# Performance work log

Hardware: AMD Instinct MI355X
Metric: run time of the kernel (lower is better)

The kernel has to match this reference:

```python
import jax, jax.numpy as jnp
import numpy as np

B, S, D, H = 2, 4096, 768, 12
DK = D // H

def setup_inputs() -> dict:
    key = jax.random.key(0)
    ks = jax.random.split(key, 11)
    scale = 1.0 / np.sqrt(D)
    inp = {
        'q': jax.random.normal(ks[0], (B, S, D), jnp.float32),
        'k': jax.random.normal(ks[1], (B, S, D), jnp.float32),
        'v': jax.random.normal(ks[2], (B, S, D), jnp.float32),
        'wq': jax.random.normal(ks[3], (D, D), jnp.float32) * scale,
        'bq': jnp.zeros((D,), jnp.float32),
        'wk': jax.random.normal(ks[4], (D, D), jnp.float32) * scale,
        'bk': jnp.zeros((D,), jnp.float32),
        'wv': jax.random.normal(ks[5], (D, D), jnp.float32) * scale,
        'bv': jnp.zeros((D,), jnp.float32),
        'wo': jax.random.normal(ks[6], (D, D), jnp.float32) * scale,
        'bo': jnp.zeros((D,), jnp.float32),
        # causal mask [S, S]; code path: 2D mask -> broadcast over batch & heads
        'mask': jnp.tril(jnp.ones((S, S), dtype=bool)),
    }
    return inp

def reference(q, k, v, wq, bq, wk, bk, wv, bv, wo, bo, mask):
    # torch Linear: y = x @ W.T + b
    def proj(x, w, b):
        # [B,S,D] -> [B,H,S,DK]
        y = jnp.einsum('bsd,ed->bse', x, w) + b
        return y.reshape(B, S, H, DK).transpose(0, 2, 1, 3)
    Q, K, V = proj(q, wq, bq), proj(k, wk, bk), proj(v, wv, bv)
    scores = jnp.einsum('bhqd,bhkd->bhqk', Q, K) / np.sqrt(DK)  # [B,H,S,S]
    scores = jnp.where(mask[None, None, :, :], scores, -1e9)
    probs = jax.nn.softmax(scores, axis=-1)
    ctx = jnp.einsum('bhqk,bhkd->bhqd', probs, V)  # [B,H,S,DK]
    ctx = ctx.transpose(0, 2, 1, 3).reshape(B, S, D)
    return jnp.einsum('bsd,ed->bse', ctx, wo) + bo
```

## Files before the change

### kernel.cpp

```cpp
#include <hip/hip_runtime.h>
#include <hip/hip_bf16.h>
#include <stdint.h>

typedef __bf16 bf16_t;
typedef __attribute__((ext_vector_type(8))) __bf16 bf16x8;
typedef __attribute__((ext_vector_type(4))) float f32x4;
typedef __attribute__((ext_vector_type(16))) float f32x16;
typedef __attribute__((ext_vector_type(2))) unsigned u32x2;

#define MFMA16(a,b,c) __builtin_amdgcn_mfma_f32_16x16x32_bf16((a),(b),(c),0,0,0)
#define MFMA32(a,b,c) __builtin_amdgcn_mfma_f32_32x32x16_bf16((a),(b),(c),0,0,0)

constexpr int BATCH = 2, SEQ = 4096, DMODEL = 768, NH = 12, DKH = 64;
constexpr int MTOT = BATCH * SEQ;
constexpr float SM_SCALE_LOG2 = 0.125f * 1.44269504088896340736f;

__device__ static inline unsigned pkbf16(float a, float b) {
    unsigned short lo = __builtin_bit_cast(unsigned short, (__bf16)a);
    unsigned short hh = __builtin_bit_cast(unsigned short, (__bf16)b);
    return ((unsigned)hh << 16) | (unsigned)lo;
}
__device__ static inline void pl32swap(unsigned& a, unsigned& b) {
    asm volatile("v_permlane32_swap_b32 %0, %1" : "+v"(a), "+v"(b));
}
__device__ static inline void gload_lds16(const void* g, void* l) {
    __builtin_amdgcn_global_load_lds((const __attribute__((address_space(1))) void*)g,
                                     (__attribute__((address_space(3))) void*)l, 16, 0, 0);
}

__global__ __launch_bounds__(256, 1)
void convert_kernel(const float* __restrict__ q, const float* __restrict__ k,
                    const float* __restrict__ v,
                    const float* __restrict__ wq, const float* __restrict__ wk,
                    const float* __restrict__ wv, const float* __restrict__ wo,
                    bf16_t* __restrict__ Xq, bf16_t* __restrict__ Xk,
                    bf16_t* __restrict__ Xv, bf16_t* __restrict__ Wb)
{
    constexpr size_t NX = (size_t)MTOT * DMODEL / 8;
    constexpr size_t NW = (size_t)DMODEL * DMODEL / 8;
    const size_t total = 3 * NX + 4 * NW;
    for (size_t u = (size_t)blockIdx.x * 256 + threadIdx.x; u < total;
         u += (size_t)gridDim.x * 256) {
        const float* src; bf16_t* dst; size_t off;
        if (u < NX)                { src = q;  dst = Xq;            off = u; }
        else if (u < 2 * NX)       { src = k;  dst = Xk;            off = u - NX; }
        else if (u < 3 * NX)       { src = v;  dst = Xv;            off = u - 2 * NX; }
        else if (u < 3 * NX + NW)      { src = wq; dst = Wb;                off = u - 3 * NX; }
        else if (u < 3 * NX + 2 * NW)  { src = wk; dst = Wb + 589824;      off = u - 3 * NX - NW; }
        else if (u < 3 * NX + 3 * NW)  { src = wv; dst = Wb + 1179648;     off = u - 3 * NX - 2 * NW; }
        else                           { src = wo; dst = Wb + 1769472;     off = u - 3 * NX - 3 * NW; }
        const float4 a = *(const float4*)(src + off * 8);
        const float4 b = *(const float4*)(src + off * 8 + 4);
        bf16x8 o;
        o[0] = (bf16_t)a.x; o[1] = (bf16_t)a.y; o[2] = (bf16_t)a.z; o[3] = (bf16_t)a.w;
        o[4] = (bf16_t)b.x; o[5] = (bf16_t)b.y; o[6] = (bf16_t)b.z; o[7] = (bf16_t)b.w;
        *(bf16x8*)(dst + off * 8) = o;
    }
}

__global__ __launch_bounds__(256, 3)
void qkv_gemm(const bf16_t* __restrict__ Xq, const bf16_t* __restrict__ Xk,
              const bf16_t* __restrict__ Xv, const bf16_t* __restrict__ Wb,
              const float* __restrict__ bq, const float* __restrict__ bk,
              const float* __restrict__ bv,
              bf16_t* __restrict__ Qp, bf16_t* __restrict__ Kp, bf16_t* __restrict__ Vp)
{
    __shared__ bf16_t SMEM[2 * 128 * 64];
    bf16_t* As = SMEM;
    bf16_t* Bs = SMEM + 8192;

    const int tid = threadIdx.x, lane = tid & 63, wave = tid >> 6;
    const int lr = lane & 15, lg = lane >> 4;
    const int wr = wave >> 1, wc = wave & 1;
    const int m0 = blockIdx.x * 128, n0 = blockIdx.y * 128;
    const int matrix = blockIdx.z;

    const bf16_t* __restrict__ X = (matrix == 0) ? Xq : (matrix == 1) ? Xk : Xv;
    const bf16_t* __restrict__ W = Wb + (size_t)matrix * 589824;

    f32x4 acc[4][4];
#pragma unroll
    for (int i = 0; i < 4; i++)
#pragma unroll
        for (int j = 0; j < 4; j++) acc[i][j] = f32x4{0.f, 0.f, 0.f, 0.f};

    const int srow = wave * 32 + (lane >> 3);
    const int schunk0 = lane & 7;

    for (int kt = 0; kt < 12; kt++) {
        const int kof = kt * 64;
#pragma unroll
        for (int i = 0; i < 4; i++) {
            const int row = srow + i * 8;
            const int sc = (schunk0 ^ (row & 7)) * 8;
            gload_lds16(X + (size_t)(m0 + row) * DMODEL + kof + sc,
                        &As[(wave * 32 + i * 8) * 64]);
            gload_lds16(W + (size_t)(n0 + row) * DMODEL + kof + sc,
                        &Bs[(wave * 32 + i * 8) * 64]);
        }
        __syncthreads();
#pragma unroll
        for (int kf = 0; kf < 2; kf++) {
            bf16x8 af[4], bfr[4];
#pragma unroll
            for (int mt = 0; mt < 4; mt++) {
                const int row = wr * 64 + mt * 16 + lr;
                af[mt] = *(const bf16x8*)&As[row * 64 + ((4 * kf + lg) ^ (lr & 7)) * 8];
            }
#pragma unroll
            for (int nt = 0; nt < 4; nt++) {
                const int row = wc * 64 + nt * 16 + lr;
                bfr[nt] = *(const bf16x8*)&Bs[row * 64 + ((4 * kf + lg) ^ (lr & 7)) * 8];
            }
#pragma unroll
            for (int mt = 0; mt < 4; mt++)
#pragma unroll
                for (int nt = 0; nt < 4; nt++)
                    acc[mt][nt] = MFMA16(af[mt], bfr[nt], acc[mt][nt]);
        }
        __syncthreads();
    }

    bf16_t* Obuf = SMEM;

    if (matrix < 2) {
        const float* bptr = (matrix == 0) ? bq : bk;
#pragma unroll
        for (int mt = 0; mt < 4; mt++) {
            const int tl = wc * 4 + 2 * wr + (mt >> 1);
            const int sl = (mt & 1) * 16 + lg * 4;
#pragma unroll
            for (int nt = 0; nt < 4; nt++) {
                const float bn = bptr[n0 + wc * 64 + nt * 16 + lr];
#pragma unroll
                for (int r = 0; r < 4; r++) {
                    const float vv = acc[mt][nt][r] + bn;
                    Obuf[tl * 2048 + (nt * 64 + ((lr >> 3) & 1) * 32 + sl + r) * 8 + (lr & 7)]
                        = (bf16_t)vv;
                }
            }
        }
    } else {
#pragma unroll
        for (int mt = 0; mt < 4; mt++) {
            const int tl = wc * 4 + 2 * wr + (mt >> 1);
#pragma unroll
            for (int nt = 0; nt < 4; nt++) {
                const float bn = bv[n0 + wc * 64 + nt * 16 + lr];
                const int c = (nt >> 1) * 2 + (mt & 1);
                const int lane_fm = (lg >> 1) * 32 + (nt & 1) * 16 + lr;
                const int e0 = (lg & 1) * 4;
#pragma unroll
                for (int r = 0; r < 4; r++) {
                    const float vv = acc[mt][nt][r] + bn;
                    Obuf[tl * 2048 + (c * 64 + lane_fm) * 8 + e0 + r] = (bf16_t)vv;
                }
            }
        }
    }
    __syncthreads();
    {
        const int tl = tid >> 5, t32 = tid & 31;
        const int hh = tl >> 2, st = tl & 3;
        const int h = (n0 + hh * 64) >> 6;
        const int mrow = m0 + st * 32;
        const int bb = mrow >> 12, s5 = (mrow & 4095) >> 5;
        bf16_t* dst = (matrix == 0 ? Qp : matrix == 1 ? Kp : Vp)
                    + (size_t)((bb * NH + h) * 128 + s5) * 2048;
        const bf16_t* srcl = Obuf + tl * 2048;
#pragma unroll
        for (int j = 0; j < 8; j++)
            *(f32x4*)(dst + (t32 + j * 32) * 8) = *(const f32x4*)(srcl + (t32 + j * 32) * 8);
    }
}

__global__ __launch_bounds__(256, 3)
void out_gemm(const bf16_t* __restrict__ Xc, const bf16_t* __restrict__ Wob,
              const float* __restrict__ bo, float* __restrict__ out)
{
    __shared__ bf16_t SMEM[2 * 128 * 64];
    bf16_t* As = SMEM;
    bf16_t* Bs = SMEM + 8192;

    const int tid = threadIdx.x, lane = tid & 63, wave = tid >> 6;
    const int lr = lane & 15, lg = lane >> 4;
    const int wr = wave >> 1, wc = wave & 1;
    const int m0 = blockIdx.x * 128, n0 = blockIdx.y * 128;

    f32x4 acc[4][4];
#pragma unroll
    for (int i = 0; i < 4; i++)
#pragma unroll
        for (int j = 0; j < 4; j++) acc[i][j] = f32x4{0.f, 0.f, 0.f, 0.f};

    const int srow = wave * 32 + (lane >> 3);
    const int schunk0 = lane & 7;

    for (int kt = 0; kt < 12; kt++) {
        const int kof = kt * 64;
#pragma unroll
        for (int i = 0; i < 4; i++) {
            const int row = srow + i * 8;
            const int sc = (schunk0 ^ (row & 7)) * 8;
            gload_lds16(Xc + (size_t)(m0 + row) * DMODEL + kof + sc,
                        &As[(wave * 32 + i * 8) * 64]);
            gload_lds16(Wob + (size_t)(n0 + row) * DMODEL + kof + sc,
                        &Bs[(wave * 32 + i * 8) * 64]);
        }
        __syncthreads();
#pragma unroll
        for (int kf = 0; kf < 2; kf++) {
            bf16x8 af[4], bfr[4];
#pragma unroll
            for (int mt = 0; mt < 4; mt++) {
                const int row = wr * 64 + mt * 16 + lr;
                af[mt] = *(const bf16x8*)&As[row * 64 + ((4 * kf + lg) ^ (lr & 7)) * 8];
            }
#pragma unroll
            for (int nt = 0; nt < 4; nt++) {
                const int row = wc * 64 + nt * 16 + lr;
                bfr[nt] = *(const bf16x8*)&Bs[row * 64 + ((4 * kf + lg) ^ (lr & 7)) * 8];
            }
#pragma unroll
            for (int mt = 0; mt < 4; mt++)
#pragma unroll
                for (int nt = 0; nt < 4; nt++)
                    acc[mt][nt] = MFMA16(af[mt], bfr[nt], acc[mt][nt]);
        }
        __syncthreads();
    }

#pragma unroll
    for (int mt = 0; mt < 4; mt++) {
#pragma unroll
        for (int nt = 0; nt < 4; nt++) {
            const int n = n0 + wc * 64 + nt * 16 + lr;
            const float bn = bo[n];
#pragma unroll
            for (int r = 0; r < 4; r++) {
                const int m = m0 + wr * 64 + mt * 16 + lg * 4 + r;
                out[(size_t)m * DMODEL + n] = acc[mt][nt][r] + bn;
            }
        }
    }
}

__global__ __launch_bounds__(256, 4)
void attn_kernel(const bf16_t* __restrict__ Qp, const bf16_t* __restrict__ Kp,
                 const bf16_t* __restrict__ Vp, bf16_t* __restrict__ ctx)
{
    __shared__ unsigned Olds[3][16][64];
    __shared__ float    Llds[3][32];

    const int tid = threadIdx.x, lane = tid & 63, wave = tid >> 6;
    const int l31 = lane & 31, hi = lane >> 5;

    const int bid = blockIdx.x;
    const int xcd = bid & 7, idx = bid >> 3;
    const int bh  = xcd * 3 + (idx >> 6);
    const int p   = idx & 63;

    const bf16_t* __restrict__ Qh = Qp + (size_t)bh * 262144;
    const bf16_t* __restrict__ Kh = Kp + (size_t)bh * 262144;
    const bf16_t* __restrict__ Vh = Vp + (size_t)bh * 262144;
    const int b = bh / NH, h = bh - (bh / NH) * NH;

    bf16x8 ones;
#pragma unroll
    for (int j = 0; j < 8; j++) ones[j] = (bf16_t)1.0f;

    for (int qs = 0; qs < 2; qs++) {
        const int qt = qs == 0 ? (127 - p) : p;
        const int qw = qt * 32;

        bf16x8 qf[4];
        {
            const bf16_t* qb = Qh + (size_t)qt * 2048 + lane * 8;
#pragma unroll
            for (int ds = 0; ds < 4; ds++) {
                bf16x8 t = *(const bf16x8*)(qb + ds * 512);
                bf16x8 sc;
#pragma unroll
                for (int j = 0; j < 8; j++) sc[j] = (bf16_t)((float)t[j] * SM_SCALE_LOG2);
                qf[ds] = sc;
            }
        }

        f32x16 oacc0, oacc1, lacc;
#pragma unroll
        for (int r = 0; r < 16; r++) { oacc0[r] = 0.f; oacc1[r] = 0.f; lacc[r] = 0.f; }

        const int ntile = qt + 1;
        for (int t = wave; t < ntile; t += 4) {
            const bf16_t* kb = Kh + (size_t)t * 2048 + lane * 8;
            bf16x8 k0 = *(const bf16x8*)(kb);
            bf16x8 k1 = *(const bf16x8*)(kb + 512);
            bf16x8 k2 = *(const bf16x8*)(kb + 1024);
            bf16x8 k3 = *(const bf16x8*)(kb + 1536);

            f32x16 s;
#pragma unroll
            for (int r = 0; r < 16; r++) s[r] = 0.f;
            s = MFMA32(k0, qf[0], s);
            s = MFMA32(k1, qf[1], s);
            s = MFMA32(k2, qf[2], s);
            s = MFMA32(k3, qf[3], s);

            const bf16_t* vb = Vh + (size_t)t * 2048 + lane * 8;
            bf16x8 v00 = *(const bf16x8*)(vb);
            bf16x8 v01 = *(const bf16x8*)(vb + 512);
            bf16x8 v10 = *(const bf16x8*)(vb + 1024);
            bf16x8 v11 = *(const bf16x8*)(vb + 1536);

            if (t == ntile - 1) {
#pragma unroll
                for (int r = 0; r < 16; r++) {
                    const int kg = (r & 3) + 8 * (r >> 2) + 4 * hi;
                    if (kg > l31) s[r] = -1e30f;
                }
            }

#pragma unroll
            for (int r = 0; r < 16; r++) s[r] = __builtin_amdgcn_exp2f(s[r]);

            union PW { unsigned w[4]; bf16x8 v; } A0, A1;
            A0.w[0] = pkbf16(s[0],  s[1]);  A0.w[1] = pkbf16(s[2],  s[3]);
            A0.w[2] = pkbf16(s[4],  s[5]);  A0.w[3] = pkbf16(s[6],  s[7]);
            pl32swap(A0.w[0], A0.w[2]);
            pl32swap(A0.w[1], A0.w[3]);
            A1.w[0] = pkbf16(s[8],  s[9]);  A1.w[1] = pkbf16(s[10], s[11]);
            A1.w[2] = pkbf16(s[12], s[13]); A1.w[3] = pkbf16(s[14], s[15]);
            pl32swap(A1.w[0], A1.w[2]);
            pl32swap(A1.w[1], A1.w[3]);

            lacc = MFMA32(ones, A0.v, lacc);
            lacc = MFMA32(ones, A1.v, lacc);

            oacc0 = MFMA32(v00, A0.v, oacc0);
            oacc0 = MFMA32(v01, A1.v, oacc0);
            oacc1 = MFMA32(v10, A0.v, oacc1);
            oacc1 = MFMA32(v11, A1.v, oacc1);
        }

        if (wave != 0) {
#pragma unroll
            for (int rp = 0; rp < 8; rp++) {
                Olds[wave - 1][rp][lane]     = pkbf16(oacc0[2 * rp], oacc0[2 * rp + 1]);
                Olds[wave - 1][8 + rp][lane] = pkbf16(oacc1[2 * rp], oacc1[2 * rp + 1]);
            }
            if (lane < 32) Llds[wave - 1][lane] = lacc[0];
        }
        __syncthreads();
        if (wave == 0) {
            const float L = lacc[0] + Llds[0][l31] + Llds[1][l31] + Llds[2][l31];
#pragma unroll
            for (int rp = 0; rp < 8; rp++) {
                unsigned u;
#pragma unroll
                for (int w = 0; w < 3; w++) {
                    u = Olds[w][rp][lane];
                    oacc0[2 * rp]     += __builtin_bit_cast(float, u << 16);
                    oacc0[2 * rp + 1] += __builtin_bit_cast(float, u & 0xffff0000u);
                    u = Olds[w][8 + rp][lane];
                    oacc1[2 * rp]     += __builtin_bit_cast(float, u << 16);
                    oacc1[2 * rp + 1] += __builtin_bit_cast(float, u & 0xffff0000u);
                }
            }
            const float rinv = 1.0f / L;
            bf16_t* orow = ctx + ((size_t)b * SEQ + qw + l31) * DMODEL + h * DKH;
#pragma unroll
            for (int g = 0; g < 4; g++) {
                {
                    u32x2 pw;
                    pw[0] = pkbf16(oacc0[g * 4 + 0] * rinv, oacc0[g * 4 + 1] * rinv);
                    pw[1] = pkbf16(oacc0[g * 4 + 2] * rinv, oacc0[g * 4 + 3] * rinv);
                    *(u32x2*)(orow + g * 8 + hi * 4) = pw;
                }
                {
                    u32x2 pw;
                    pw[0] = pkbf16(oacc1[g * 4 + 0] * rinv, oacc1[g * 4 + 1] * rinv);
                    pw[1] = pkbf16(oacc1[g * 4 + 2] * rinv, oacc1[g * 4 + 3] * rinv);
                    *(u32x2*)(orow + 32 + g * 8 + hi * 4) = pw;
                }
            }
        }
        __syncthreads();
    }
}

extern "C" void kernel_launch(void* const* d_in, const int* in_sizes, int n_in,
                              void* d_out, int out_size, void* d_ws, size_t ws_size,
                              hipStream_t stream)
{
    const float* q   = (const float*)d_in[0];
    const float* kin = (const float*)d_in[1];
    const float* vin = (const float*)d_in[2];
    const float* wq  = (const float*)d_in[3];
    const float* bq  = (const float*)d_in[4];
    const float* wk  = (const float*)d_in[5];
    const float* bk  = (const float*)d_in[6];
    const float* wv  = (const float*)d_in[7];
    const float* bv  = (const float*)d_in[8];
    const float* wo  = (const float*)d_in[9];
    const float* bo  = (const float*)d_in[10];

    const size_t per = (size_t)BATCH * NH * SEQ * DKH;
    bf16_t* Qp  = (bf16_t*)d_ws;
    bf16_t* Kp  = Qp + per;
    bf16_t* Vp  = Kp + per;
    bf16_t* ctx = Vp + per;
    bf16_t* Xq  = ctx + per;
    bf16_t* Xk  = Xq + per;
    bf16_t* Xv  = Xk + per;
    bf16_t* Wb  = Xv + per;

    convert_kernel<<<dim3(2048), dim3(256), 0, stream>>>(q, kin, vin, wq, wk, wv, wo,
                                                         Xq, Xk, Xv, Wb);

    qkv_gemm<<<dim3(MTOT / 128, DMODEL / 128, 3), dim3(256), 0, stream>>>(
        Xq, Xk, Xv, Wb, bq, bk, bv, Qp, Kp, Vp);

    attn_kernel<<<dim3(1536), dim3(256), 0, stream>>>(Qp, Kp, Vp, ctx);

    out_gemm<<<dim3(MTOT / 128, DMODEL / 128), dim3(256), 0, stream>>>(
        ctx, Wb + (size_t)3 * DMODEL * DMODEL, bo, (float*)d_out);
}
```

Baseline: 163.5 us.

## Assign one query tile per wave and share LDS-staged K/V across waves

```diff
diff --git a/kernel.cpp b/kernel.cpp
--- a/kernel.cpp
+++ b/kernel.cpp
@@ -249,50 +249,60 @@
 void attn_kernel(const bf16_t* __restrict__ Qp, const bf16_t* __restrict__ Kp,
                  const bf16_t* __restrict__ Vp, bf16_t* __restrict__ ctx)
 {
-    __shared__ unsigned Olds[3][16][64];
-    __shared__ float    Llds[3][32];
+    __shared__ bf16_t Kl[2][2048];
+    __shared__ bf16_t Vl[2][2048];
 
     const int tid = threadIdx.x, lane = tid & 63, wave = tid >> 6;
     const int l31 = lane & 31, hi = lane >> 5;
 
     const int bid = blockIdx.x;
     const int xcd = bid & 7, idx = bid >> 3;
-    const int bh  = xcd * 3 + (idx >> 6);
-    const int p   = idx & 63;
+    const int bh  = xcd * 3 + (idx >> 5);
+    const int u   = 31 - (idx & 31);
+    const int qt  = 4 * u + wave;
+    const int qw  = qt * 32;
 
     const bf16_t* __restrict__ Qh = Qp + (size_t)bh * 262144;
     const bf16_t* __restrict__ Kh = Kp + (size_t)bh * 262144;
     const bf16_t* __restrict__ Vh = Vp + (size_t)bh * 262144;
     const int b = bh / NH, h = bh - (bh / NH) * NH;
 
+    bf16x8 qf[4];
+    {
+        const bf16_t* qb = Qh + (size_t)qt * 2048 + lane * 8;
+#pragma unroll
+        for (int ds = 0; ds < 4; ds++) {
+            bf16x8 t = *(const bf16x8*)(qb + ds * 512);
+            bf16x8 sc;
+#pragma unroll
+            for (int j = 0; j < 8; j++) sc[j] = (bf16_t)((float)t[j] * SM_SCALE_LOG2);
+            qf[ds] = sc;
+        }
+    }
+
     bf16x8 ones;
 #pragma unroll
     for (int j = 0; j < 8; j++) ones[j] = (bf16_t)1.0f;
 
-    for (int qs = 0; qs < 2; qs++) {
-        const int qt = qs == 0 ? (127 - p) : p;
-        const int qw = qt * 32;
-
-        bf16x8 qf[4];
-        {
-            const bf16_t* qb = Qh + (size_t)qt * 2048 + lane * 8;
-#pragma unroll
-            for (int ds = 0; ds < 4; ds++) {
-                bf16x8 t = *(const bf16x8*)(qb + ds * 512);
-                bf16x8 sc;
-#pragma unroll
-                for (int j = 0; j < 8; j++) sc[j] = (bf16_t)((float)t[j] * SM_SCALE_LOG2);
-                qf[ds] = sc;
-            }
-        }
-
-        f32x16 oacc0, oacc1, lacc;
-#pragma unroll
-        for (int r = 0; r < 16; r++) { oacc0[r] = 0.f; oacc1[r] = 0.f; lacc[r] = 0.f; }
-
-        const int ntile = qt + 1;
-        for (int t = wave; t < ntile; t += 4) {
-            const bf16_t* kb = Kh + (size_t)t * 2048 + lane * 8;
+    f32x16 oacc0, oacc1, lacc;
+#pragma unroll
+    for (int r = 0; r < 16; r++) { oacc0[r] = 0.f; oacc1[r] = 0.f; lacc[r] = 0.f; }
+
+    auto stage = [&](int buf, int t) {
+        gload_lds16(Kh + (size_t)t * 2048 + tid * 8, &Kl[buf][wave * 512]);
+        gload_lds16(Vh + (size_t)t * 2048 + tid * 8, &Vl[buf][wave * 512]);
+    };
+
+    const int T = 4 * u + 4;
+    stage(0, 0);
+    __syncthreads();
+
+    for (int t = 0; t < T; t++) {
+        const int cur = t & 1;
+        if (t + 1 < T) stage(cur ^ 1, t + 1);
+
+        if (t <= qt) {
+            const bf16_t* kb = &Kl[cur][lane * 8];
             bf16x8 k0 = *(const bf16x8*)(kb);
             bf16x8 k1 = *(const bf16x8*)(kb + 512);
             bf16x8 k2 = *(const bf16x8*)(kb + 1024);
@@ -306,13 +316,13 @@
             s = MFMA32(k2, qf[2], s);
             s = MFMA32(k3, qf[3], s);
 
-            const bf16_t* vb = Vh + (size_t)t * 2048 + lane * 8;
+            const bf16_t* vb = &Vl[cur][lane * 8];
             bf16x8 v00 = *(const bf16x8*)(vb);
             bf16x8 v01 = *(const bf16x8*)(vb + 512);
             bf16x8 v10 = *(const bf16x8*)(vb + 1024);
             bf16x8 v11 = *(const bf16x8*)(vb + 1536);
 
-            if (t == ntile - 1) {
+            if (t == qt) {
 #pragma unroll
                 for (int r = 0; r < 16; r++) {
                     const int kg = (r & 3) + 8 * (r >> 2) + 4 * hi;
@@ -341,50 +351,25 @@
             oacc1 = MFMA32(v10, A0.v, oacc1);
             oacc1 = MFMA32(v11, A1.v, oacc1);
         }
-
-        if (wave != 0) {
-#pragma unroll
-            for (int rp = 0; rp < 8; rp++) {
-                Olds[wave - 1][rp][lane]     = pkbf16(oacc0[2 * rp], oacc0[2 * rp + 1]);
-                Olds[wave - 1][8 + rp][lane] = pkbf16(oacc1[2 * rp], oacc1[2 * rp + 1]);
-            }
-            if (lane < 32) Llds[wave - 1][lane] = lacc[0];
-        }
         __syncthreads();
-        if (wave == 0) {
-            const float L = lacc[0] + Llds[0][l31] + Llds[1][l31] + Llds[2][l31];
-#pragma unroll
-            for (int rp = 0; rp < 8; rp++) {
-                unsigned u;
-#pragma unroll
-                for (int w = 0; w < 3; w++) {
-                    u = Olds[w][rp][lane];
-                    oacc0[2 * rp]     += __builtin_bit_cast(float, u << 16);
-                    oacc0[2 * rp + 1] += __builtin_bit_cast(float, u & 0xffff0000u);
-                    u = Olds[w][8 + rp][lane];
-                    oacc1[2 * rp]     += __builtin_bit_cast(float, u << 16);
-                    oacc1[2 * rp + 1] += __builtin_bit_cast(float, u & 0xffff0000u);
-                }
-            }
-            const float rinv = 1.0f / L;
-            bf16_t* orow = ctx + ((size_t)b * SEQ + qw + l31) * DMODEL + h * DKH;
-#pragma unroll
-            for (int g = 0; g < 4; g++) {
-                {
-                    u32x2 pw;
-                    pw[0] = pkbf16(oacc0[g * 4 + 0] * rinv, oacc0[g * 4 + 1] * rinv);
-                    pw[1] = pkbf16(oacc0[g * 4 + 2] * rinv, oacc0[g * 4 + 3] * rinv);
-                    *(u32x2*)(orow + g * 8 + hi * 4) = pw;
-                }
-                {
-                    u32x2 pw;
-                    pw[0] = pkbf16(oacc1[g * 4 + 0] * rinv, oacc1[g * 4 + 1] * rinv);
-                    pw[1] = pkbf16(oacc1[g * 4 + 2] * rinv, oacc1[g * 4 + 3] * rinv);
-                    *(u32x2*)(orow + 32 + g * 8 + hi * 4) = pw;
-                }
-            }
-        }
-        __syncthreads();
+    }
+
+    const float rinv = 1.0f / lacc[0];
+    bf16_t* orow = ctx + ((size_t)b * SEQ + qw + l31) * DMODEL + h * DKH;
+#pragma unroll
+    for (int g = 0; g < 4; g++) {
+        {
+            u32x2 pw;
+            pw[0] = pkbf16(oacc0[g * 4 + 0] * rinv, oacc0[g * 4 + 1] * rinv);
+            pw[1] = pkbf16(oacc0[g * 4 + 2] * rinv, oacc0[g * 4 + 3] * rinv);
+            *(u32x2*)(orow + g * 8 + hi * 4) = pw;
+        }
+        {
+            u32x2 pw;
+            pw[0] = pkbf16(oacc1[g * 4 + 0] * rinv, oacc1[g * 4 + 1] * rinv);
+            pw[1] = pkbf16(oacc1[g * 4 + 2] * rinv, oacc1[g * 4 + 3] * rinv);
+            *(u32x2*)(orow + 32 + g * 8 + hi * 4) = pw;
+        }
     }
 }
 
@@ -420,7 +405,7 @@
     qkv_gemm<<<dim3(MTOT / 128, DMODEL / 128, 3), dim3(256), 0, stream>>>(
         Xq, Xk, Xv, Wb, bq, bk, bv, Qp, Kp, Vp);
 
-    attn_kernel<<<dim3(1536), dim3(256), 0, stream>>>(Qp, Kp, Vp, ctx);
+    attn_kernel<<<dim3(768), dim3(256), 0, stream>>>(Qp, Kp, Vp, ctx);
 
     out_gemm<<<dim3(MTOT / 128, DMODEL / 128), dim3(256), 0, stream>>>(
         ctx, Wb + (size_t)3 * DMODEL * DMODEL, bo, (float*)d_out);
```

Measured after the change: 198.9 us. 21.7% more time.

## Process two adjacent query tiles per block to reuse K/V loads

Applied to the files above, without the earlier changes.

```diff
diff --git a/kernel.cpp b/kernel.cpp
--- a/kernel.cpp
+++ b/kernel.cpp
@@ -245,66 +245,78 @@
     }
 }
 
-__global__ __launch_bounds__(256, 4)
+__global__ __launch_bounds__(256, 3)
 void attn_kernel(const bf16_t* __restrict__ Qp, const bf16_t* __restrict__ Kp,
                  const bf16_t* __restrict__ Vp, bf16_t* __restrict__ ctx)
 {
-    __shared__ unsigned Olds[3][16][64];
-    __shared__ float    Llds[3][32];
+    __shared__ unsigned Olds[3][32][64];
+    __shared__ float    Llds[3][2][32];
 
     const int tid = threadIdx.x, lane = tid & 63, wave = tid >> 6;
     const int l31 = lane & 31, hi = lane >> 5;
 
     const int bid = blockIdx.x;
     const int xcd = bid & 7, idx = bid >> 3;
-    const int bh  = xcd * 3 + (idx >> 6);
-    const int p   = idx & 63;
+    const int bh  = xcd * 3 + (idx >> 5);
+    const int g   = idx & 31;
 
     const bf16_t* __restrict__ Qh = Qp + (size_t)bh * 262144;
     const bf16_t* __restrict__ Kh = Kp + (size_t)bh * 262144;
     const bf16_t* __restrict__ Vh = Vp + (size_t)bh * 262144;
     const int b = bh / NH, h = bh - (bh / NH) * NH;
 
-    bf16x8 ones;
-#pragma unroll
-    for (int j = 0; j < 8; j++) ones[j] = (bf16_t)1.0f;
-
-    for (int qs = 0; qs < 2; qs++) {
-        const int qt = qs == 0 ? (127 - p) : p;
-        const int qw = qt * 32;
-
-        bf16x8 qf[4];
+    for (int ph = 0; ph < 2; ph++) {
+        const int p  = (ph == 0) ? (63 - g) : g;
+        const int qa = 2 * p, qb = 2 * p + 1;
+
+        bf16x8 qfA[4], qfB[4];
         {
-            const bf16_t* qb = Qh + (size_t)qt * 2048 + lane * 8;
+            const bf16_t* qba = Qh + (size_t)qa * 2048 + lane * 8;
 #pragma unroll
             for (int ds = 0; ds < 4; ds++) {
-                bf16x8 t = *(const bf16x8*)(qb + ds * 512);
-                bf16x8 sc;
-#pragma unroll
-                for (int j = 0; j < 8; j++) sc[j] = (bf16_t)((float)t[j] * SM_SCALE_LOG2);
-                qf[ds] = sc;
-            }
-        }
-
-        f32x16 oacc0, oacc1, lacc;
-#pragma unroll
-        for (int r = 0; r < 16; r++) { oacc0[r] = 0.f; oacc1[r] = 0.f; lacc[r] = 0.f; }
-
-        const int ntile = qt + 1;
-        for (int t = wave; t < ntile; t += 4) {
+                bf16x8 t0 = *(const bf16x8*)(qba + ds * 512);
+                bf16x8 t1 = *(const bf16x8*)(qba + 2048 + ds * 512);
+                bf16x8 s0, s1;
+#pragma unroll
+                for (int j = 0; j < 8; j++) {
+                    s0[j] = (bf16_t)((float)t0[j] * SM_SCALE_LOG2);
+                    s1[j] = (bf16_t)((float)t1[j] * SM_SCALE_LOG2);
+                }
+                qfA[ds] = s0; qfB[ds] = s1;
+            }
+        }
+
+        f32x16 oA0, oA1, oB0, oB1;
+#pragma unroll
+        for (int r = 0; r < 16; r++) { oA0[r] = 0.f; oA1[r] = 0.f; oB0[r] = 0.f; oB1[r] = 0.f; }
+        float lA = 0.f, lB = 0.f;
+
+        for (int t = wave; t <= qb; t += 4) {
             const bf16_t* kb = Kh + (size_t)t * 2048 + lane * 8;
             bf16x8 k0 = *(const bf16x8*)(kb);
             bf16x8 k1 = *(const bf16x8*)(kb + 512);
             bf16x8 k2 = *(const bf16x8*)(kb + 1024);
             bf16x8 k3 = *(const bf16x8*)(kb + 1536);
 
-            f32x16 s;
-#pragma unroll
-            for (int r = 0; r < 16; r++) s[r] = 0.f;
-            s = MFMA32(k0, qf[0], s);
-            s = MFMA32(k1, qf[1], s);
-            s = MFMA32(k2, qf[2], s);
-            s = MFMA32(k3, qf[3], s);
+            const bool actA = (t <= qa);
+
+            f32x16 sB;
+#pragma unroll
+            for (int r = 0; r < 16; r++) sB[r] = 0.f;
+            sB = MFMA32(k0, qfB[0], sB);
+            sB = MFMA32(k1, qfB[1], sB);
+            sB = MFMA32(k2, qfB[2], sB);
+            sB = MFMA32(k3, qfB[3], sB);
+
+            f32x16 sA;
+#pragma unroll
+            for (int r = 0; r < 16; r++) sA[r] = 0.f;
+            if (actA) {
+                sA = MFMA32(k0, qfA[0], sA);
+                sA = MFMA32(k1, qfA[1], sA);
+                sA = MFMA32(k2, qfA[2], sA);
+                sA = MFMA32(k3, qfA[3], sA);
+            }
 
             const bf16_t* vb = Vh + (size_t)t * 2048 + lane * 8;
             bf16x8 v00 = *(const bf16x8*)(vb);
@@ -312,76 +324,118 @@
             bf16x8 v10 = *(const bf16x8*)(vb + 1024);
             bf16x8 v11 = *(const bf16x8*)(vb + 1536);
 
-            if (t == ntile - 1) {
+            if (t == qa) {
 #pragma unroll
                 for (int r = 0; r < 16; r++) {
                     const int kg = (r & 3) + 8 * (r >> 2) + 4 * hi;
-                    if (kg > l31) s[r] = -1e30f;
-                }
-            }
-
-#pragma unroll
-            for (int r = 0; r < 16; r++) s[r] = __builtin_amdgcn_exp2f(s[r]);
-
-            union PW { unsigned w[4]; bf16x8 v; } A0, A1;
-            A0.w[0] = pkbf16(s[0],  s[1]);  A0.w[1] = pkbf16(s[2],  s[3]);
-            A0.w[2] = pkbf16(s[4],  s[5]);  A0.w[3] = pkbf16(s[6],  s[7]);
-            pl32swap(A0.w[0], A0.w[2]);
-            pl32swap(A0.w[1], A0.w[3]);
-            A1.w[0] = pkbf16(s[8],  s[9]);  A1.w[1] = pkbf16(s[10], s[11]);
-            A1.w[2] = pkbf16(s[12], s[13]); A1.w[3] = pkbf16(s[14], s[15]);
-            pl32swap(A1.w[0], A1.w[2]);
-            pl32swap(A1.w[1], A1.w[3]);
-
-            lacc = MFMA32(ones, A0.v, lacc);
-            lacc = MFMA32(ones, A1.v, lacc);
-
-            oacc0 = MFMA32(v00, A0.v, oacc0);
-            oacc0 = MFMA32(v01, A1.v, oacc0);
-            oacc1 = MFMA32(v10, A0.v, oacc1);
-            oacc1 = MFMA32(v11, A1.v, oacc1);
+                    if (kg > l31) sA[r] = -1e30f;
+                }
+            }
+            if (t == qb) {
+#pragma unroll
+                for (int r = 0; r < 16; r++) {
+                    const int kg = (r & 3) + 8 * (r >> 2) + 4 * hi;
+                    if (kg > l31) sB[r] = -1e30f;
+                }
+            }
+
+            {
+                float ps = 0.f;
+#pragma unroll
+                for (int r = 0; r < 16; r++) {
+                    sB[r] = __builtin_amdgcn_exp2f(sB[r]);
+                    ps += sB[r];
+                }
+                lB += ps + __shfl_xor(ps, 32);
+                union PW { unsigned w[4]; bf16x8 v; } B0, B1;
+                B0.w[0] = pkbf16(sB[0],  sB[1]);  B0.w[1] = pkbf16(sB[2],  sB[3]);
+                B0.w[2] = pkbf16(sB[4],  sB[5]);  B0.w[3] = pkbf16(sB[6],  sB[7]);
+                pl32swap(B0.w[0], B0.w[2]);
+                pl32swap(B0.w[1], B0.w[3]);
+                B1.w[0] = pkbf16(sB[8],  sB[9]);  B1.w[1] = pkbf16(sB[10], sB[11]);
+                B1.w[2] = pkbf16(sB[12], sB[13]); B1.w[3] = pkbf16(sB[14], sB[15]);
+                pl32swap(B1.w[0], B1.w[2]);
+                pl32swap(B1.w[1], B1.w[3]);
+                oB0 = MFMA32(v00, B0.v, oB0);
+                oB0 = MFMA32(v01, B1.v, oB0);
+                oB1 = MFMA32(v10, B0.v, oB1);
+                oB1 = MFMA32(v11, B1.v, oB1);
+            }
+            if (actA) {
+                float ps = 0.f;
+#pragma unroll
+                for (int r = 0; r < 16; r++) {
+                    sA[r] = __builtin_amdgcn_exp2f(sA[r]);
+                    ps += sA[r];
+                }
+                lA += ps + __shfl_xor(ps, 32);
+                union PW { unsigned w[4]; bf16x8 v; } A0, A1;
+                A0.w[0] = pkbf16(sA[0],  sA[1]);  A0.w[1] = pkbf16(sA[2],  sA[3]);
+                A0.w[2] = pkbf16(sA[4],  sA[5]);  A0.w[3] = pkbf16(sA[6],  sA[7]);
+                pl32swap(A0.w[0], A0.w[2]);
+                pl32swap(A0.w[1], A0.w[3]);
+                A1.w[0] = pkbf16(sA[8],  sA[9]);  A1.w[1] = pkbf16(sA[10], sA[11]);
+                A1.w[2] = pkbf16(sA[12], sA[13]); A1.w[3] = pkbf16(sA[14], sA[15]);
+                pl32swap(A1.w[0], A1.w[2]);
+                pl32swap(A1.w[1], A1.w[3]);
+                oA0 = MFMA32(v00, A0.v, oA0);
+                oA0 = MFMA32(v01, A1.v, oA0);
+                oA1 = MFMA32(v10, A0.v, oA1);
+                oA1 = MFMA32(v11, A1.v, oA1);
+            }
         }
 
         if (wave != 0) {
 #pragma unroll
             for (int rp = 0; rp < 8; rp++) {
-                Olds[wave - 1][rp][lane]     = pkbf16(oacc0[2 * rp], oacc0[2 * rp + 1]);
-                Olds[wave - 1][8 + rp][lane] = pkbf16(oacc1[2 * rp], oacc1[2 * rp + 1]);
-            }
-            if (lane < 32) Llds[wave - 1][lane] = lacc[0];
+                Olds[wave - 1][rp][lane]      = pkbf16(oA0[2 * rp], oA0[2 * rp + 1]);
+                Olds[wave - 1][8 + rp][lane]  = pkbf16(oA1[2 * rp], oA1[2 * rp + 1]);
+                Olds[wave - 1][16 + rp][lane] = pkbf16(oB0[2 * rp], oB0[2 * rp + 1]);
+                Olds[wave - 1][24 + rp][lane] = pkbf16(oB1[2 * rp], oB1[2 * rp + 1]);
+            }
+            if (lane < 32) { Llds[wave - 1][0][lane] = lA; Llds[wave - 1][1][lane] = lB; }
         }
         __syncthreads();
         if (wave == 0) {
-            const float L = lacc[0] + Llds[0][l31] + Llds[1][l31] + Llds[2][l31];
+            const float LA = lA + Llds[0][0][l31] + Llds[1][0][l31] + Llds[2][0][l31];
+            const float LB = lB + Llds[0][1][l31] + Llds[1][1][l31] + Llds[2][1][l31];
 #pragma unroll
             for (int rp = 0; rp < 8; rp++) {
                 unsigned u;
 #pragma unroll
                 for (int w = 0; w < 3; w++) {
                     u = Olds[w][rp][lane];
-                    oacc0[2 * rp]     += __builtin_bit_cast(float, u << 16);
-                    oacc0[2 * rp + 1] += __builtin_bit_cast(float, u & 0xffff0000u);
+                    oA0[2 * rp]     += __builtin_bit_cast(float, u << 16);
+                    oA0[2 * rp + 1] += __builtin_bit_cast(float, u & 0xffff0000u);
                     u = Olds[w][8 + rp][lane];
-                    oacc1[2 * rp]     += __builtin_bit_cast(float, u << 16);
-                    oacc1[2 * rp + 1] += __builtin_bit_cast(float, u & 0xffff0000u);
-                }
-            }
-            const float rinv = 1.0f / L;
-            bf16_t* orow = ctx + ((size_t)b * SEQ + qw + l31) * DMODEL + h * DKH;
-#pragma unroll
-            for (int g = 0; g < 4; g++) {
-                {
-                    u32x2 pw;
-                    pw[0] = pkbf16(oacc0[g * 4 + 0] * rinv, oacc0[g * 4 + 1] * rinv);
-                    pw[1] = pkbf16(oacc0[g * 4 + 2] * rinv, oacc0[g * 4 + 3] * rinv);
-                    *(u32x2*)(orow + g * 8 + hi * 4) = pw;
-                }
-                {
-                    u32x2 pw;
-                    pw[0] = pkbf16(oacc1[g * 4 + 0] * rinv, oacc1[g * 4 + 1] * rinv);
-                    pw[1] = pkbf16(oacc1[g * 4 + 2] * rinv, oacc1[g * 4 + 3] * rinv);
-                    *(u32x2*)(orow + 32 + g * 8 + hi * 4) = pw;
-                }
+                    oA1[2 * rp]     += __builtin_bit_cast(float, u << 16);
+                    oA1[2 * rp + 1] += __builtin_bit_cast(float, u & 0xffff0000u);
+                    u = Olds[w][16 + rp][lane];
+                    oB0[2 * rp]     += __builtin_bit_cast(float, u << 16);
+                    oB0[2 * rp + 1] += __builtin_bit_cast(float, u & 0xffff0000u);
+                    u = Olds[w][24 + rp][lane];
+                    oB1[2 * rp]     += __builtin_bit_cast(float, u << 16);
+                    oB1[2 * rp + 1] += __builtin_bit_cast(float, u & 0xffff0000u);
+                }
+            }
+            const float rA = 1.0f / LA, rB = 1.0f / LB;
+            bf16_t* orA = ctx + ((size_t)b * SEQ + qa * 32 + l31) * DMODEL + h * DKH;
+            bf16_t* orB = ctx + ((size_t)b * SEQ + qb * 32 + l31) * DMODEL + h * DKH;
+#pragma unroll
+            for (int gq = 0; gq < 4; gq++) {
+                u32x2 pw;
+                pw[0] = pkbf16(oA0[gq * 4 + 0] * rA, oA0[gq * 4 + 1] * rA);
+                pw[1] = pkbf16(oA0[gq * 4 + 2] * rA, oA0[gq * 4 + 3] * rA);
+                *(u32x2*)(orA + gq * 8 + hi * 4) = pw;
+                pw[0] = pkbf16(oA1[gq * 4 + 0] * rA, oA1[gq * 4 + 1] * rA);
+                pw[1] = pkbf16(oA1[gq * 4 + 2] * rA, oA1[gq * 4 + 3] * rA);
+                *(u32x2*)(orA + 32 + gq * 8 + hi * 4) = pw;
+                pw[0] = pkbf16(oB0[gq * 4 + 0] * rB, oB0[gq * 4 + 1] * rB);
+                pw[1] = pkbf16(oB0[gq * 4 + 2] * rB, oB0[gq * 4 + 3] * rB);
+                *(u32x2*)(orB + gq * 8 + hi * 4) = pw;
+                pw[0] = pkbf16(oB1[gq * 4 + 0] * rB, oB1[gq * 4 + 1] * rB);
+                pw[1] = pkbf16(oB1[gq * 4 + 2] * rB, oB1[gq * 4 + 3] * rB);
+                *(u32x2*)(orB + 32 + gq * 8 + hi * 4) = pw;
             }
         }
         __syncthreads();
@@ -420,7 +474,7 @@
     qkv_gemm<<<dim3(MTOT / 128, DMODEL / 128, 3), dim3(256), 0, stream>>>(
         Xq, Xk, Xv, Wb, bq, bk, bv, Qp, Kp, Vp);
 
-    attn_kernel<<<dim3(1536), dim3(256), 0, stream>>>(Qp, Kp, Vp, ctx);
+    attn_kernel<<<dim3(768), dim3(256), 0, stream>>>(Qp, Kp, Vp, ctx);
 
     out_gemm<<<dim3(MTOT / 128, DMODEL / 128), dim3(256), 0, stream>>>(
         ctx, Wb + (size_t)3 * DMODEL * DMODEL, bo, (float*)d_out);
```

Result: slower. 167.1 us (+2.2%).

## Fuse fp32-to-bf16 activation conversion into QKV GEMM A-operand loads

Applied to the files above, without the earlier changes.

```diff
diff --git a/kernel.cpp b/kernel.cpp
--- a/kernel.cpp
+++ b/kernel.cpp
@@ -29,26 +29,19 @@
 }
 
 __global__ __launch_bounds__(256, 1)
-void convert_kernel(const float* __restrict__ q, const float* __restrict__ k,
-                    const float* __restrict__ v,
-                    const float* __restrict__ wq, const float* __restrict__ wk,
+void convert_kernel(const float* __restrict__ wq, const float* __restrict__ wk,
                     const float* __restrict__ wv, const float* __restrict__ wo,
-                    bf16_t* __restrict__ Xq, bf16_t* __restrict__ Xk,
-                    bf16_t* __restrict__ Xv, bf16_t* __restrict__ Wb)
+                    bf16_t* __restrict__ Wb)
 {
-    constexpr size_t NX = (size_t)MTOT * DMODEL / 8;
     constexpr size_t NW = (size_t)DMODEL * DMODEL / 8;
-    const size_t total = 3 * NX + 4 * NW;
+    const size_t total = 4 * NW;
     for (size_t u = (size_t)blockIdx.x * 256 + threadIdx.x; u < total;
          u += (size_t)gridDim.x * 256) {
         const float* src; bf16_t* dst; size_t off;
-        if (u < NX)                { src = q;  dst = Xq;            off = u; }
-        else if (u < 2 * NX)       { src = k;  dst = Xk;            off = u - NX; }
-        else if (u < 3 * NX)       { src = v;  dst = Xv;            off = u - 2 * NX; }
-        else if (u < 3 * NX + NW)      { src = wq; dst = Wb;                off = u - 3 * NX; }
-        else if (u < 3 * NX + 2 * NW)  { src = wk; dst = Wb + 589824;      off = u - 3 * NX - NW; }
-        else if (u < 3 * NX + 3 * NW)  { src = wv; dst = Wb + 1179648;     off = u - 3 * NX - 2 * NW; }
-        else                           { src = wo; dst = Wb + 1769472;     off = u - 3 * NX - 3 * NW; }
+        if (u < NW)          { src = wq; dst = Wb;           off = u; }
+        else if (u < 2 * NW) { src = wk; dst = Wb + 589824;  off = u - NW; }
+        else if (u < 3 * NW) { src = wv; dst = Wb + 1179648; off = u - 2 * NW; }
+        else                 { src = wo; dst = Wb + 1769472; off = u - 3 * NW; }
         const float4 a = *(const float4*)(src + off * 8);
         const float4 b = *(const float4*)(src + off * 8 + 4);
         bf16x8 o;
@@ -59,15 +52,14 @@
 }
 
 __global__ __launch_bounds__(256, 3)
-void qkv_gemm(const bf16_t* __restrict__ Xq, const bf16_t* __restrict__ Xk,
-              const bf16_t* __restrict__ Xv, const bf16_t* __restrict__ Wb,
+void qkv_gemm(const float* __restrict__ Xq, const float* __restrict__ Xk,
+              const float* __restrict__ Xv, const bf16_t* __restrict__ Wb,
               const float* __restrict__ bq, const float* __restrict__ bk,
               const float* __restrict__ bv,
               bf16_t* __restrict__ Qp, bf16_t* __restrict__ Kp, bf16_t* __restrict__ Vp)
 {
-    __shared__ bf16_t SMEM[2 * 128 * 64];
-    bf16_t* As = SMEM;
-    bf16_t* Bs = SMEM + 8192;
+    __shared__ bf16_t SMEM[16384];
+    bf16_t* Bs = SMEM;
 
     const int tid = threadIdx.x, lane = tid & 63, wave = tid >> 6;
     const int lr = lane & 15, lg = lane >> 4;
@@ -75,7 +67,7 @@
     const int m0 = blockIdx.x * 128, n0 = blockIdx.y * 128;
     const int matrix = blockIdx.z;
 
-    const bf16_t* __restrict__ X = (matrix == 0) ? Xq : (matrix == 1) ? Xk : Xv;
+    const float*  __restrict__ X = (matrix == 0) ? Xq : (matrix == 1) ? Xk : Xv;
     const bf16_t* __restrict__ W = Wb + (size_t)matrix * 589824;
 
     f32x4 acc[4][4];
@@ -93,8 +85,6 @@
         for (int i = 0; i < 4; i++) {
             const int row = srow + i * 8;
             const int sc = (schunk0 ^ (row & 7)) * 8;
-            gload_lds16(X + (size_t)(m0 + row) * DMODEL + kof + sc,
-                        &As[(wave * 32 + i * 8) * 64]);
             gload_lds16(W + (size_t)(n0 + row) * DMODEL + kof + sc,
                         &Bs[(wave * 32 + i * 8) * 64]);
         }
@@ -104,8 +94,14 @@
             bf16x8 af[4], bfr[4];
 #pragma unroll
             for (int mt = 0; mt < 4; mt++) {
-                const int row = wr * 64 + mt * 16 + lr;
-                af[mt] = *(const bf16x8*)&As[row * 64 + ((4 * kf + lg) ^ (lr & 7)) * 8];
+                const float* ap = X + (size_t)(m0 + wr * 64 + mt * 16 + lr) * DMODEL
+                                    + kof + kf * 32 + lg * 8;
+                const float4 a0 = *(const float4*)ap;
+                const float4 a1 = *(const float4*)(ap + 4);
+                bf16x8 t;
+                t[0] = (bf16_t)a0.x; t[1] = (bf16_t)a0.y; t[2] = (bf16_t)a0.z; t[3] = (bf16_t)a0.w;
+                t[4] = (bf16_t)a1.x; t[5] = (bf16_t)a1.y; t[6] = (bf16_t)a1.z; t[7] = (bf16_t)a1.w;
+                af[mt] = t;
             }
 #pragma unroll
             for (int nt = 0; nt < 4; nt++) {
@@ -409,16 +405,12 @@
     bf16_t* Kp  = Qp + per;
     bf16_t* Vp  = Kp + per;
     bf16_t* ctx = Vp + per;
-    bf16_t* Xq  = ctx + per;
-    bf16_t* Xk  = Xq + per;
-    bf16_t* Xv  = Xk + per;
-    bf16_t* Wb  = Xv + per;
-
-    convert_kernel<<<dim3(2048), dim3(256), 0, stream>>>(q, kin, vin, wq, wk, wv, wo,
-                                                         Xq, Xk, Xv, Wb);
+    bf16_t* Wb  = ctx + per;
+
+    convert_kernel<<<dim3(1152), dim3(256), 0, stream>>>(wq, wk, wv, wo, Wb);
 
     qkv_gemm<<<dim3(MTOT / 128, DMODEL / 128, 3), dim3(256), 0, stream>>>(
-        Xq, Xk, Xv, Wb, bq, bk, bv, Qp, Kp, Vp);
+        q, kin, vin, Wb, bq, bk, bv, Qp, Kp, Vp);
 
     attn_kernel<<<dim3(1536), dim3(256), 0, stream>>>(Qp, Kp, Vp, ctx);
 
```

Result: slower. 245.6 us (+50.3%).
